# Performance work log

Measured on AMD Instinct MI355X. Metric: run time of the kernel, lower is better.

Reference implementation:

```python
import jax, jax.numpy as jnp
import numpy as np

EXP_ORDER = 2  # matches init_kwargs exp_order
N_FEAT = 8
Q_DIM = 1
BATCH = 262144
T_EXPANDED = 164  # n + C(n+1,2) + C(n+2,3) for n=8, degrees 1..3
N_OUT = 8


def taylor_expand(x, exp_order):
    """Faithful vectorized version of the nested multiply/concat loop.

    x: [B, n, q]. Builds all monomials of degree 1..exp_order+1 using the same
    recursion as the TF code: at each order, for each j, multiply x_j with the
    previous-order block starting at Id[j], then append. The q-loop in the
    original is replaced by broadcasting over the q axis (identical math).
    """
    n = x.shape[1]
    Id = list(range(n))  # start index of x_j's block in the previous-order terms
    epd = x
    for _ in range(exp_order):
        L = epd.shape[1]  # slice end Id[n-1]+1 always equals current length
        blocks = []
        new_Id = []
        offset = L
        for j in range(n):
            blk = x[:, j:j + 1, :] * epd[:, Id[j]:L, :]  # [B, L-Id[j], q]
            new_Id.append(offset)
            offset += blk.shape[1]
            blocks.append(blk)
        epd = jnp.concatenate([epd] + blocks, axis=1)
        Id = new_Id
    return epd


def setup_inputs() -> dict:
    key = jax.random.key(0)
    k1, k2, k3 = jax.random.split(key, 3)
    x = jax.random.normal(k1, (BATCH, N_FEAT, Q_DIM), dtype=jnp.float32)
    # 'dl' init: uniform(-1/sqrt(fan), 1/sqrt(fan)) with fan = weights_shape[0]
    dl_scale = 1.0 / np.sqrt(N_OUT)
    W = jax.random.uniform(k2, (N_OUT, T_EXPANDED), minval=-dl_scale,
                           maxval=dl_scale, dtype=jnp.float32)
    # 'uniform' bias init: U(-0.2, 0.2), shape [out, 1]
    b = jax.random.uniform(k3, (N_OUT, 1), minval=-0.2, maxval=0.2,
                           dtype=jnp.float32)
    return {"x": x, "W": W, "b": b}


def reference(x, W, b):
    # cp_type == 'none': pass-through of the input
    epd = taylor_expand(x, EXP_ORDER)          # [B, T, q]
    out = jnp.einsum('ot,btq->boq', W, epd) + b[None]  # [B, out, q]
    # act_type == 'relu'
    return jax.nn.relu(out)
```

## Files before the change

### kernel.cpp

```cpp
#include <hip/hip_runtime.h>
#include <hip/hip_bf16.h>
#include <string.h>


static constexpr int TEXP = 164;
static constexpr int NOUT = 8;
static constexpr int NMFMA = 11;
static constexpr int NSLOT = 88;
static constexpr int BIAS_T = 200;
static constexpr int NWP = NMFMA * 64 * 8;

using f32x16 = __attribute__((ext_vector_type(16))) float;
using short8 = __attribute__((ext_vector_type(8))) short;

constexpr int rowstart2(int j) { return j * 8 - j * (j - 1) / 2; }
constexpr int start3(int j) {
  int s = 44;
  for (int jp = 0; jp < j; ++jp) s += (8 - jp) * (9 - jp) / 2;
  return s;
}
constexpr int t3_of(int a, int b, int c) {
  int x = a, y = b, z = c, t = 0;
  if (x > y) { t = x; x = y; y = t; }
  if (y > z) { t = y; y = z; z = t; }
  if (x > y) { t = x; x = y; y = t; }
  int off = 0;
  for (int ap = x; ap < y; ++ap) off += 8 - ap;
  return start3(x) + off + (z - y);
}

struct Slot { int deg, a, b, c; };
struct SlotTable { Slot s[NSLOT]; };

constexpr bool isrep2(int j, int k) {
  if (k < 4) return true;
  if (j >= 4) return false;
  if (k == j + 4) return true;
  return j < k - 4;
}
constexpr bool isrep3(int a, int b, int c) {
  return ((a < 4) + (b < 4) + (c < 4)) >= 2;
}

constexpr SlotTable make_slots() {
  SlotTable T{};
  int s = 0;
  for (int j = 0; j < 4; ++j) T.s[s++] = {1, j, 0, 0};
  for (int j = 0; j < 8; ++j)
    for (int k = j; k < 8; ++k)
      if (isrep2(j, k)) T.s[s++] = {2, j, k, 0};
  for (int a = 0; a < 8; ++a)
    for (int b = a; b < 8; ++b)
      for (int c = b; c < 8; ++c)
        if (isrep3(a, b, c)) T.s[s++] = {3, a, b, c};
  for (; s < NSLOT; ++s) T.s[s] = {0, 0, 0, 0};
  return T;
}
constexpr SlotTable SLOTS = make_slots();

struct TT { short t[2][NSLOT]; };
constexpr TT make_tt() {
  TT r{};
  for (int h = 0; h < 2; ++h)
    for (int s = 0; s < NSLOT; ++s) {
      Slot sl = SLOTS.s[s];
      int m = h ? 4 : 0;
      if (sl.deg == 0) {
        r.t[h][s] = (short)((h == 0 && s == 84) ? BIAS_T : -1);
      } else if (sl.deg == 1) {
        r.t[h][s] = (short)(sl.a ^ m);
      } else if (sl.deg == 2) {
        if (h == 1 && sl.b == (sl.a ^ 4)) { r.t[h][s] = -1; }
        else {
          int a = sl.a ^ m, b = sl.b ^ m;
          int lo = a < b ? a : b, hi2 = a < b ? b : a;
          r.t[h][s] = (short)(8 + rowstart2(lo) + (hi2 - lo));
        }
      } else {
        r.t[h][s] = (short)t3_of(sl.a ^ m, sl.b ^ m, sl.c ^ m);
      }
    }
  return r;
}
__device__ const TT TDX = make_tt();

__device__ __forceinline__ unsigned short bf16rne(float v) {
  union { float f; unsigned int u; } c; c.f = v;
  unsigned int u = c.u;
  return (unsigned short)((u + 0x7fffu + ((u >> 16) & 1u)) >> 16);
}

template <int S>
__device__ __forceinline__ float slotval(const float (&xs)[8], const float (&d2)[26]) {
  constexpr int deg = SLOTS.s[S].deg;
  constexpr int a = SLOTS.s[S].a;
  constexpr int b = SLOTS.s[S].b;
  constexpr int c = SLOTS.s[S].c;
  if constexpr (deg == 1) return xs[a];
  else if constexpr (deg == 2) return d2[rowstart2(a) + (b - a)];
  else if constexpr (deg == 3) return xs[a] * d2[rowstart2(b) + (c - b)];
  else if constexpr (S == 84) return 1.0f;
  else return 0.0f;
}

template <int I>
struct MfmaStep {
  static __device__ __forceinline__ void run(const float (&xs)[8], const float (&d2)[26],
                                             const unsigned short* __restrict__ wpl,
                                             short8 af_cur, f32x16& acc) {
    short8 af_next;
    if constexpr (I + 1 < NMFMA)
      af_next = *reinterpret_cast<const short8*>(wpl + (I + 1) * 64 * 8);
    short8 bv;
    bv[0] = (short)bf16rne(slotval<8 * I + 0>(xs, d2));
    bv[1] = (short)bf16rne(slotval<8 * I + 1>(xs, d2));
    bv[2] = (short)bf16rne(slotval<8 * I + 2>(xs, d2));
    bv[3] = (short)bf16rne(slotval<8 * I + 3>(xs, d2));
    bv[4] = (short)bf16rne(slotval<8 * I + 4>(xs, d2));
    bv[5] = (short)bf16rne(slotval<8 * I + 5>(xs, d2));
    bv[6] = (short)bf16rne(slotval<8 * I + 6>(xs, d2));
    bv[7] = (short)bf16rne(slotval<8 * I + 7>(xs, d2));
    acc = __builtin_amdgcn_mfma_f32_32x32x16_bf16(af_cur, bv, acc, 0, 0, 0);
    if constexpr (I + 1 < NMFMA)
      MfmaStep<I + 1>::run(xs, d2, wpl, af_next, acc);
  }
};

__device__ __forceinline__ void chain(const float (&xs)[8],
                                      const unsigned short* __restrict__ wpl,
                                      float* __restrict__ dst) {
  float d2[26];
#pragma unroll
  for (int j = 0; j < 4; ++j) {
#pragma unroll
    for (int k = j; k < 8; ++k) {
      d2[rowstart2(j) + (k - j)] = xs[j] * xs[k];
    }
  }
  short8 af0 = *reinterpret_cast<const short8*>(wpl);
  f32x16 acc;
#pragma unroll
  for (int r = 0; r < 16; ++r) acc[r] = 0.0f;
  MfmaStep<0>::run(xs, d2, wpl, af0, acc);
  float4 o;
  o.x = fmaxf(acc[0], 0.0f);
  o.y = fmaxf(acc[1], 0.0f);
  o.z = fmaxf(acc[2], 0.0f);
  o.w = fmaxf(acc[3], 0.0f);
  *reinterpret_cast<float4*>(dst) = o;
}

__global__ void prep_w(const float* __restrict__ W, const float* __restrict__ b,
                       unsigned short* __restrict__ wp) {
  int idx = threadIdx.x + blockIdx.x * blockDim.x;
  if (idx >= NWP) return;
  int j = idx & 7;
  int lane = (idx >> 3) & 63;
  int i = idx >> 9;
  int row = lane & 31, h = lane >> 5;
  int t = TDX.t[h][8 * i + j];
  float v = 0.0f;
  if (row < NOUT) {
    if (t >= 0 && t < TEXP) v = W[row * TEXP + t];
    else if (t == BIAS_T) v = b[row];
  }
  wp[idx] = bf16rne(v);
}

__global__ __launch_bounds__(256, 4) void taylor_mfma(
    const float* __restrict__ x, const unsigned short* __restrict__ wp,
    float* __restrict__ out, int ngroups) {
  const int lane = (int)(threadIdx.x & 63);
  const int h = (lane >= 32) ? 1 : 0;
  const int col = lane & 31;

  const int wave = (int)((blockIdx.x * blockDim.x + threadIdx.x) >> 6);
  const int g0 = wave * 2;
  if (g0 >= ngroups) return;

  const int elem0 = g0 * 32 + col;
  const int elem1 = elem0 + 32;

  const float* xe0 = x + elem0 * 8;
  const float* xe1 = x + elem1 * 8;
  float4 a0 = *reinterpret_cast<const float4*>(xe0 + 4 * h);
  float4 b0 = *reinterpret_cast<const float4*>(xe0 + 4 - 4 * h);
  float4 a1 = *reinterpret_cast<const float4*>(xe1 + 4 * h);
  float4 b1 = *reinterpret_cast<const float4*>(xe1 + 4 - 4 * h);

  const unsigned short* wpl = wp + lane * 8;

  float xs0[8] = {a0.x, a0.y, a0.z, a0.w, b0.x, b0.y, b0.z, b0.w};
  chain(xs0, wpl, out + elem0 * 8 + 4 * h);

  float xs1[8] = {a1.x, a1.y, a1.z, a1.w, b1.x, b1.y, b1.z, b1.w};
  chain(xs1, wpl, out + elem1 * 8 + 4 * h);
}

extern "C" void kernel_launch(void* const* d_in, const int* in_sizes, int n_in,
                              void* d_out, int out_size, void* d_ws, size_t ws_size,
                              hipStream_t stream) {
  const float* x = (const float*)d_in[0];
  const float* W = (const float*)d_in[1];
  const float* b = (const float*)d_in[2];
  float* out = (float*)d_out;
  unsigned short* wp = (unsigned short*)d_ws;

  int n = in_sizes[0] / 8;
  int ngroups = n / 32;
  int blocks = ngroups / 8;

  prep_w<<<22, 256, 0, stream>>>(W, b, wp);
  taylor_mfma<<<blocks, 256, 0, stream>>>(x, wp, out, ngroups);
}
```

Baseline: 17.25 us.

## Switch to 16x16x32 MFMA with four-way symmetric monomial split across lane quarters

Replaces the 32x32x16 MFMA chain (11 steps, 88 slots, two half-wave permutations) with a 16x16x32 chain (6 steps, 48 slots) that exploits a four-way XOR-permutation symmetry of the features. Each lane quarter holds a permuted copy of x, and duplicate monomials are masked out in the weight table. The goal is fewer MFMA steps and less per-lane monomial and bf16 conversion work, with a higher occupancy hint. In exchange half the lanes do no stores, the inputs are loaded as float2 pieces, and the hardware bf16 cast is used instead of manual rounding.

```diff
diff --git a/kernel.cpp b/kernel.cpp
--- a/kernel.cpp
+++ b/kernel.cpp
@@ -5,12 +5,13 @@
 
 static constexpr int TEXP = 164;
 static constexpr int NOUT = 8;
-static constexpr int NMFMA = 11;
-static constexpr int NSLOT = 88;
+static constexpr int NMFMA = 6;
+static constexpr int NSLOT = 48;
+static constexpr int NPAIR = 12;
 static constexpr int BIAS_T = 200;
 static constexpr int NWP = NMFMA * 64 * 8;
 
-using f32x16 = __attribute__((ext_vector_type(16))) float;
+using f32x4 = __attribute__((ext_vector_type(4))) float;
 using short8 = __attribute__((ext_vector_type(8))) short;
 
 constexpr int rowstart2(int j) { return j * 8 - j * (j - 1) / 2; }
@@ -29,56 +30,62 @@
   return start3(x) + off + (z - y);
 }
 
-struct Slot { int deg, a, b, c; };
-struct SlotTable { Slot s[NSLOT]; };
-
-constexpr bool isrep2(int j, int k) {
-  if (k < 4) return true;
-  if (j >= 4) return false;
-  if (k == j + 4) return true;
-  return j < k - 4;
-}
-constexpr bool isrep3(int a, int b, int c) {
-  return ((a < 4) + (b < 4) + (c < 4)) >= 2;
-}
-
-constexpr SlotTable make_slots() {
-  SlotTable T{};
-  int s = 0;
-  for (int j = 0; j < 4; ++j) T.s[s++] = {1, j, 0, 0};
-  for (int j = 0; j < 8; ++j)
-    for (int k = j; k < 8; ++k)
-      if (isrep2(j, k)) T.s[s++] = {2, j, k, 0};
-  for (int a = 0; a < 8; ++a)
-    for (int b = a; b < 8; ++b)
-      for (int c = b; c < 8; ++c)
-        if (isrep3(a, b, c)) T.s[s++] = {3, a, b, c};
-  for (; s < NSLOT; ++s) T.s[s] = {0, 0, 0, 0};
-  return T;
-}
-constexpr SlotTable SLOTS = make_slots();
-
-struct TT { short t[2][NSLOT]; };
+constexpr int PAIRA[NPAIR] = {0,1,0,1,0,1,0,1,0,0,0,0};
+constexpr int PAIRB[NPAIR] = {0,1,2,3,4,5,6,7,1,3,5,7};
+
+struct Prog { int kind, a, p; };
+constexpr Prog PRG[NSLOT] = {
+  {0,0,0},{0,1,0},
+  {1,0,0},{1,0,1},{1,0,2},{1,0,3},{1,0,4},{1,0,5},
+  {1,0,6},{1,0,7},{1,0,8},{1,0,9},{1,0,10},{1,0,11},
+  {2,0,0},{2,2,0},{2,4,0},{2,6,0},{2,4,2},
+  {2,1,1},{2,3,1},{2,5,1},{2,7,1},{2,5,3},
+  {2,1,0},{2,3,0},{2,5,0},{2,7,0},{2,2,8},{2,2,10},{2,4,8},{2,4,9},{2,6,8},{2,6,9},
+  {2,1,8},{2,3,8},{2,5,8},{2,7,8},{2,3,9},{2,5,9},{2,7,9},{2,5,10},{2,7,10},{2,7,11},
+  {3,0,0},
+  {4,0,0},{4,0,0},{4,0,0}
+};
+
+struct MS { int n; int v[3]; };
+constexpr MS slot_ms(int s, int q) {
+  Prog g = PRG[s];
+  int m = 2 * q;
+  MS r{0, {0,0,0}};
+  if (g.kind == 0) { r.n = 1; r.v[0] = g.a ^ m; }
+  else if (g.kind == 1) { r.n = 2; r.v[0] = PAIRA[g.p] ^ m; r.v[1] = PAIRB[g.p] ^ m; }
+  else if (g.kind == 2) {
+    r.n = 3; r.v[0] = g.a ^ m; r.v[1] = PAIRA[g.p] ^ m; r.v[2] = PAIRB[g.p] ^ m;
+  }
+  for (int i = 0; i < r.n; ++i)
+    for (int j = i + 1; j < r.n; ++j)
+      if (r.v[j] < r.v[i]) { int t = r.v[i]; r.v[i] = r.v[j]; r.v[j] = t; }
+  return r;
+}
+constexpr bool ms_eq(MS a, MS b) {
+  if (a.n != b.n || a.n == 0) return false;
+  for (int i = 0; i < a.n; ++i) if (a.v[i] != b.v[i]) return false;
+  return true;
+}
+constexpr int ms_t(MS a) {
+  if (a.n == 1) return a.v[0];
+  if (a.n == 2) return 8 + rowstart2(a.v[0]) + (a.v[1] - a.v[0]);
+  if (a.n == 3) return t3_of(a.v[0], a.v[1], a.v[2]);
+  return -1;
+}
+
+struct TT { short t[4][NSLOT]; };
 constexpr TT make_tt() {
   TT r{};
-  for (int h = 0; h < 2; ++h)
+  for (int q = 0; q < 4; ++q)
     for (int s = 0; s < NSLOT; ++s) {
-      Slot sl = SLOTS.s[s];
-      int m = h ? 4 : 0;
-      if (sl.deg == 0) {
-        r.t[h][s] = (short)((h == 0 && s == 84) ? BIAS_T : -1);
-      } else if (sl.deg == 1) {
-        r.t[h][s] = (short)(sl.a ^ m);
-      } else if (sl.deg == 2) {
-        if (h == 1 && sl.b == (sl.a ^ 4)) { r.t[h][s] = -1; }
-        else {
-          int a = sl.a ^ m, b = sl.b ^ m;
-          int lo = a < b ? a : b, hi2 = a < b ? b : a;
-          r.t[h][s] = (short)(8 + rowstart2(lo) + (hi2 - lo));
-        }
-      } else {
-        r.t[h][s] = (short)t3_of(sl.a ^ m, sl.b ^ m, sl.c ^ m);
-      }
+      Prog g = PRG[s];
+      if (g.kind == 3) { r.t[q][s] = (short)(q == 0 ? BIAS_T : -1); continue; }
+      if (g.kind == 4) { r.t[q][s] = -1; continue; }
+      MS ms = slot_ms(s, q);
+      bool dup = false;
+      for (int q2 = 0; q2 < q; ++q2)
+        if (ms_eq(slot_ms(s, q2), ms)) dup = true;
+      r.t[q][s] = (short)(dup ? -1 : ms_t(ms));
     }
   return r;
 }
@@ -89,65 +96,71 @@
   unsigned int u = c.u;
   return (unsigned short)((u + 0x7fffu + ((u >> 16) & 1u)) >> 16);
 }
+__device__ __forceinline__ short bf16cast(float v) {
+  __hip_bfloat16 h = __float2bfloat16(v);
+  short s;
+  memcpy(&s, &h, 2);
+  return s;
+}
 
 template <int S>
-__device__ __forceinline__ float slotval(const float (&xs)[8], const float (&d2)[26]) {
-  constexpr int deg = SLOTS.s[S].deg;
-  constexpr int a = SLOTS.s[S].a;
-  constexpr int b = SLOTS.s[S].b;
-  constexpr int c = SLOTS.s[S].c;
-  if constexpr (deg == 1) return xs[a];
-  else if constexpr (deg == 2) return d2[rowstart2(a) + (b - a)];
-  else if constexpr (deg == 3) return xs[a] * d2[rowstart2(b) + (c - b)];
-  else if constexpr (S == 84) return 1.0f;
+__device__ __forceinline__ float slotval(const float (&xs)[8], const float (&p)[NPAIR]) {
+  constexpr Prog g = PRG[S];
+  if constexpr (g.kind == 0) return xs[g.a];
+  else if constexpr (g.kind == 1) return p[g.p];
+  else if constexpr (g.kind == 2) return xs[g.a] * p[g.p];
+  else if constexpr (g.kind == 3) return 1.0f;
   else return 0.0f;
 }
 
 template <int I>
 struct MfmaStep {
-  static __device__ __forceinline__ void run(const float (&xs)[8], const float (&d2)[26],
+  static __device__ __forceinline__ void run(const float (&xs)[8], const float (&p)[NPAIR],
                                              const unsigned short* __restrict__ wpl,
-                                             short8 af_cur, f32x16& acc) {
+                                             short8 af_cur, f32x4& acc) {
     short8 af_next;
     if constexpr (I + 1 < NMFMA)
       af_next = *reinterpret_cast<const short8*>(wpl + (I + 1) * 64 * 8);
     short8 bv;
-    bv[0] = (short)bf16rne(slotval<8 * I + 0>(xs, d2));
-    bv[1] = (short)bf16rne(slotval<8 * I + 1>(xs, d2));
-    bv[2] = (short)bf16rne(slotval<8 * I + 2>(xs, d2));
-    bv[3] = (short)bf16rne(slotval<8 * I + 3>(xs, d2));
-    bv[4] = (short)bf16rne(slotval<8 * I + 4>(xs, d2));
-    bv[5] = (short)bf16rne(slotval<8 * I + 5>(xs, d2));
-    bv[6] = (short)bf16rne(slotval<8 * I + 6>(xs, d2));
-    bv[7] = (short)bf16rne(slotval<8 * I + 7>(xs, d2));
-    acc = __builtin_amdgcn_mfma_f32_32x32x16_bf16(af_cur, bv, acc, 0, 0, 0);
+    bv[0] = bf16cast(slotval<8 * I + 0>(xs, p));
+    bv[1] = bf16cast(slotval<8 * I + 1>(xs, p));
+    bv[2] = bf16cast(slotval<8 * I + 2>(xs, p));
+    bv[3] = bf16cast(slotval<8 * I + 3>(xs, p));
+    bv[4] = bf16cast(slotval<8 * I + 4>(xs, p));
+    bv[5] = bf16cast(slotval<8 * I + 5>(xs, p));
+    bv[6] = bf16cast(slotval<8 * I + 6>(xs, p));
+    bv[7] = bf16cast(slotval<8 * I + 7>(xs, p));
+    acc = __builtin_amdgcn_mfma_f32_16x16x32_bf16(af_cur, bv, acc, 0, 0, 0);
     if constexpr (I + 1 < NMFMA)
-      MfmaStep<I + 1>::run(xs, d2, wpl, af_next, acc);
+      MfmaStep<I + 1>::run(xs, p, wpl, af_next, acc);
   }
 };
 
-__device__ __forceinline__ void chain(const float (&xs)[8],
+__device__ __forceinline__ void chain(const float* __restrict__ xe, int q,
                                       const unsigned short* __restrict__ wpl,
-                                      float* __restrict__ dst) {
-  float d2[26];
+                                      float* __restrict__ dst, bool st) {
+  float2 B0 = *reinterpret_cast<const float2*>(xe + ((0 ^ q) * 2));
+  float2 B1 = *reinterpret_cast<const float2*>(xe + ((1 ^ q) * 2));
+  float2 B2 = *reinterpret_cast<const float2*>(xe + ((2 ^ q) * 2));
+  float2 B3 = *reinterpret_cast<const float2*>(xe + ((3 ^ q) * 2));
+  float xs[8] = {B0.x, B0.y, B1.x, B1.y, B2.x, B2.y, B3.x, B3.y};
+
+  float p[NPAIR];
 #pragma unroll
-  for (int j = 0; j < 4; ++j) {
-#pragma unroll
-    for (int k = j; k < 8; ++k) {
-      d2[rowstart2(j) + (k - j)] = xs[j] * xs[k];
-    }
-  }
+  for (int i = 0; i < NPAIR; ++i) p[i] = xs[PAIRA[i]] * xs[PAIRB[i]];
+
   short8 af0 = *reinterpret_cast<const short8*>(wpl);
-  f32x16 acc;
-#pragma unroll
-  for (int r = 0; r < 16; ++r) acc[r] = 0.0f;
-  MfmaStep<0>::run(xs, d2, wpl, af0, acc);
-  float4 o;
-  o.x = fmaxf(acc[0], 0.0f);
-  o.y = fmaxf(acc[1], 0.0f);
-  o.z = fmaxf(acc[2], 0.0f);
-  o.w = fmaxf(acc[3], 0.0f);
-  *reinterpret_cast<float4*>(dst) = o;
+  f32x4 acc = {0.0f, 0.0f, 0.0f, 0.0f};
+  MfmaStep<0>::run(xs, p, wpl, af0, acc);
+
+  if (st) {
+    float4 o;
+    o.x = fmaxf(acc[0], 0.0f);
+    o.y = fmaxf(acc[1], 0.0f);
+    o.z = fmaxf(acc[2], 0.0f);
+    o.w = fmaxf(acc[3], 0.0f);
+    *reinterpret_cast<float4*>(dst) = o;
+  }
 }
 
 __global__ void prep_w(const float* __restrict__ W, const float* __restrict__ b,
@@ -157,8 +170,8 @@
   int j = idx & 7;
   int lane = (idx >> 3) & 63;
   int i = idx >> 9;
-  int row = lane & 31, h = lane >> 5;
-  int t = TDX.t[h][8 * i + j];
+  int row = lane & 15, q = lane >> 4;
+  int t = TDX.t[q][8 * i + j];
   float v = 0.0f;
   if (row < NOUT) {
     if (t >= 0 && t < TEXP) v = W[row * TEXP + t];
@@ -167,34 +180,23 @@
   wp[idx] = bf16rne(v);
 }
 
-__global__ __launch_bounds__(256, 4) void taylor_mfma(
+__global__ __launch_bounds__(256, 8) void taylor_mfma(
     const float* __restrict__ x, const unsigned short* __restrict__ wp,
-    float* __restrict__ out, int ngroups) {
+    float* __restrict__ out) {
   const int lane = (int)(threadIdx.x & 63);
-  const int h = (lane >= 32) ? 1 : 0;
-  const int col = lane & 31;
+  const int q = lane >> 4;
+  const int col = lane & 15;
+  const bool st = q < 2;
+  const int ro = (q & 1) * 4;
 
   const int wave = (int)((blockIdx.x * blockDim.x + threadIdx.x) >> 6);
-  const int g0 = wave * 2;
-  if (g0 >= ngroups) return;
-
-  const int elem0 = g0 * 32 + col;
-  const int elem1 = elem0 + 32;
-
-  const float* xe0 = x + elem0 * 8;
-  const float* xe1 = x + elem1 * 8;
-  float4 a0 = *reinterpret_cast<const float4*>(xe0 + 4 * h);
-  float4 b0 = *reinterpret_cast<const float4*>(xe0 + 4 - 4 * h);
-  float4 a1 = *reinterpret_cast<const float4*>(xe1 + 4 * h);
-  float4 b1 = *reinterpret_cast<const float4*>(xe1 + 4 - 4 * h);
+  const int elem0 = wave * 32 + col;
+  const int elem1 = elem0 + 16;
 
   const unsigned short* wpl = wp + lane * 8;
 
-  float xs0[8] = {a0.x, a0.y, a0.z, a0.w, b0.x, b0.y, b0.z, b0.w};
-  chain(xs0, wpl, out + elem0 * 8 + 4 * h);
-
-  float xs1[8] = {a1.x, a1.y, a1.z, a1.w, b1.x, b1.y, b1.z, b1.w};
-  chain(xs1, wpl, out + elem1 * 8 + 4 * h);
+  chain(x + elem0 * 8, q, wpl, out + elem0 * 8 + ro, st);
+  chain(x + elem1 * 8, q, wpl, out + elem1 * 8 + ro, st);
 }
 
 extern "C" void kernel_launch(void* const* d_in, const int* in_sizes, int n_in,
@@ -207,9 +209,8 @@
   unsigned short* wp = (unsigned short*)d_ws;
 
   int n = in_sizes[0] / 8;
-  int ngroups = n / 32;
-  int blocks = ngroups / 8;
-
-  prep_w<<<22, 256, 0, stream>>>(W, b, wp);
-  taylor_mfma<<<blocks, 256, 0, stream>>>(x, wp, out, ngroups);
-}
+  int blocks = n / 128;
+
+  prep_w<<<12, 256, 0, stream>>>(W, b, wp);
+  taylor_mfma<<<blocks, 256, 0, stream>>>(x, wp, out);
+}
```

Measured after the change: 16.73 us. -3.0%, faster.
